# Kernel optimization log

Measured on AMD Instinct MI355X. Metric: run time of the kernel, lower is better.

The kernel has to match this reference:

```python
import jax, jax.numpy as jnp
import numpy as np

B, S, D = 2, 2048, 2048
H, HKV, DH = 32, 8, 64
WIN = 1024  # sliding_window
SCALE = 1.0 / np.sqrt(DH)
NEG_INF = -1e30


def setup_inputs() -> dict:
    key = jax.random.key(0)
    ks = jax.random.split(key, 6)
    w = 0.02
    inp = {
        "hidden_states": jax.random.normal(ks[0], (B, S, D), jnp.float32),
        "Wq": jax.random.normal(ks[1], (D, D), jnp.float32) * w,
        "bq": jnp.zeros((D,), jnp.float32),
        "Wk": jax.random.normal(ks[2], (HKV * DH, D), jnp.float32) * w,
        "bk": jnp.zeros((HKV * DH,), jnp.float32),
        "Wv": jax.random.normal(ks[3], (HKV * DH, D), jnp.float32) * w,
        "bv": jnp.zeros((HKV * DH,), jnp.float32),
        "Wo": jax.random.normal(ks[4], (D, D), jnp.float32) * w,
        "bo": jnp.zeros((D,), jnp.float32),
        # reset_parameters (default init): 1 / logspace(0, 7, H, base=2)
        "alibi_slopes": 1.0 / jnp.exp2(jnp.linspace(0.0, 7.0, H)).astype(jnp.float32),
    }
    return inp


def reference(hidden_states, Wq, bq, Wk, bk, Wv, bv, Wo, bo, alibi_slopes):
    x = hidden_states
    q = (x @ Wq.T + bq).reshape(B, S, H, DH).transpose(0, 2, 1, 3)      # [B,H,S,DH]
    k = (x @ Wk.T + bk).reshape(B, S, HKV, DH).transpose(0, 2, 1, 3)    # [B,HKV,S,DH]
    v = (x @ Wv.T + bv).reshape(B, S, HKV, DH).transpose(0, 2, 1, 3)
    # GQA: each kv head serves H//HKV consecutive query heads
    group = H // HKV
    k = jnp.repeat(k, group, axis=1)  # [B,H,S,DH]
    v = jnp.repeat(v, group, axis=1)

    scores = jnp.einsum("bhqd,bhkd->bhqk", q, k) * SCALE  # [B,H,S,S]
    i = jnp.arange(S)[:, None]
    j = jnp.arange(S)[None, :]
    rel = (j - i).astype(jnp.float32)  # <= 0 for attended past positions
    # ALiBi: slope * (j - i) -> linear penalty on distance
    bias = alibi_slopes[:, None, None] * rel  # [H,S,S]
    mask = (j <= i) & ((i - j) < WIN)  # [S,S]
    scores = jnp.where(mask[None, None], scores + bias[None], NEG_INF)
    probs = jax.nn.softmax(scores, axis=-1)
    out = jnp.einsum("bhqk,bhkd->bhqd", probs, v)  # [B,H,S,DH]
    out = out.transpose(0, 2, 1, 3).reshape(B, S, D)
    return out @ Wo.T + bo
```

## Files before the change

### kernel.cpp

```cpp
#include <hip/hip_runtime.h>
#include <hip/hip_bf16.h>
#include <stdint.h>
#include <type_traits>

typedef unsigned short ushort_t;
typedef __bf16 bf16x8 __attribute__((ext_vector_type(8)));
typedef __bf16 bf16x4 __attribute__((ext_vector_type(4)));
typedef short s16x4 __attribute__((ext_vector_type(4)));
typedef unsigned short u16x8 __attribute__((ext_vector_type(8)));
typedef float f32x4 __attribute__((ext_vector_type(4)));

#define MFMA_BF16(a, b, c) __builtin_amdgcn_mfma_f32_16x16x32_bf16((a), (b), (c), 0, 0, 0)

#define GLD_LDS(gptr, lptr) \
    __builtin_amdgcn_global_load_lds((const __attribute__((address_space(1))) void*)(gptr), \
                                     (__attribute__((address_space(3))) void*)(lptr), 16, 0, 0)

static __device__ __forceinline__ float bf2f(__hip_bfloat16 x) { return __bfloat162float(x); }
static __device__ __forceinline__ ushort_t f2bfbits(float f) {
    __hip_bfloat16 h = __float2bfloat16(f);
    return *(ushort_t*)&h;
}
static __device__ __forceinline__ float fmax3(float a, float b, float c) {
    return fmaxf(fmaxf(a, b), c);
}

static __device__ __forceinline__ f32x4 MFMA16(bf16x4 a, bf16x4 b, f32x4 c) {
#if __has_builtin(__builtin_amdgcn_mfma_f32_16x16x16_bf16)
    return __builtin_amdgcn_mfma_f32_16x16x16_bf16(a, b, c, 0, 0, 0);
#elif __has_builtin(__builtin_amdgcn_mfma_f32_16x16x16bf16_1k)
    union { bf16x4 b4; s16x4 s4; } ua, ub;
    ua.b4 = a; ub.b4 = b;
    return __builtin_amdgcn_mfma_f32_16x16x16bf16_1k(ua.s4, ub.s4, c, 0, 0, 0);
#else
    const bf16x4 z = {(__bf16)0.f, (__bf16)0.f, (__bf16)0.f, (__bf16)0.f};
    bf16x8 a8 = __builtin_shufflevector(a, z, 0, 1, 2, 3, 4, 5, 6, 7);
    bf16x8 b8 = __builtin_shufflevector(b, z, 0, 1, 2, 3, 4, 5, 6, 7);
    return MFMA_BF16(a8, b8, c);
#endif
}

static __device__ __forceinline__ bf16x4 pack4(float a, float b, float c, float d) {
    union { ushort4 u; bf16x4 v; } r;
    r.u = make_ushort4(f2bfbits(a), f2bfbits(b), f2bfbits(c), f2bfbits(d));
    return r.v;
}

template <typename T>
static __device__ __forceinline__ void storeT(T* p, float v);
template <>
__device__ __forceinline__ void storeT<float>(float* p, float v) { *p = v; }
template <>
__device__ __forceinline__ void storeT<__hip_bfloat16>(__hip_bfloat16* p, float v) {
    *p = __float2bfloat16(v);
}

__global__ void detect_kernel(const ushort_t* __restrict__ X,
                              const void* bq, const void* bk, const void* bv,
                              const void* bo, const void* slopes,
                              int* flag, float* slopesF, float* bqF,
                              float* bkF, float* bvF, float* boF) {
    __shared__ int cnt_s;
    if (threadIdx.x == 0) cnt_s = 0;
    __syncthreads();
    int cnt = 0;
    for (int i = threadIdx.x; i < 8192; i += 256) {
        ushort_t u = X[2 * i];
        int ex = (u >> 7) & 0xFF;
        if (ex >= 0xC0) cnt++;
    }
    for (int off = 1; off < 64; off <<= 1) cnt += __shfl_xor(cnt, off);
    if ((threadIdx.x & 63) == 0) atomicAdd(&cnt_s, cnt);
    __syncthreads();
    const bool f32 = cnt_s > 100;
    if (threadIdx.x == 0) *flag = f32 ? 1 : 0;
    auto conv = [&](const void* src, float* dst, int n) {
        for (int i = threadIdx.x; i < n; i += 256)
            dst[i] = f32 ? ((const float*)src)[i]
                         : __bfloat162float(((const __hip_bfloat16*)src)[i]);
    };
    conv(bq, bqF, 2048);
    conv(bk, bkF, 512);
    conv(bv, bvF, 512);
    conv(bo, boF, 2048);
    conv(slopes, slopesF, 32);
}

__global__ __launch_bounds__(256) void cvt_kernel(const int* __restrict__ flag,
                                                  const void* __restrict__ src,
                                                  ushort_t* __restrict__ dst, int n4) {
    const bool f32 = (*flag == 1);
    const int stride = gridDim.x * 256;
    for (int i = blockIdx.x * 256 + threadIdx.x; i < n4; i += stride) {
        if (f32) {
            float4 f = ((const float4*)src)[i];
            ((ushort4*)dst)[i] =
                make_ushort4(f2bfbits(f.x), f2bfbits(f.y), f2bfbits(f.z), f2bfbits(f.w));
        } else {
            ((ushort4*)dst)[i] = ((const ushort4*)src)[i];
        }
    }
}

__global__ __launch_bounds__(256) void cvt4_kernel(const int* __restrict__ flag,
                                                   const void* __restrict__ X,
                                                   const void* __restrict__ Wq,
                                                   const void* __restrict__ Wk,
                                                   const void* __restrict__ Wv,
                                                   ushort_t* __restrict__ Xb,
                                                   ushort_t* __restrict__ Wqb,
                                                   ushort_t* __restrict__ Wkb,
                                                   ushort_t* __restrict__ Wvb) {
    const bool f32 = (*flag == 1);
    constexpr int nX = 4096 * 2048 / 4;
    constexpr int nWq = 2048 * 2048 / 4;
    constexpr int nWk = 512 * 2048 / 4;
    constexpr int total = nX + nWq + 2 * nWk;
    const int stride = gridDim.x * 256;
    for (int i = blockIdx.x * 256 + threadIdx.x; i < total; i += stride) {
        const void* src;
        ushort_t* dst;
        int off;
        if (i < nX)                 { src = X;  dst = Xb;  off = i; }
        else if (i < nX + nWq)      { src = Wq; dst = Wqb; off = i - nX; }
        else if (i < nX + nWq + nWk){ src = Wk; dst = Wkb; off = i - nX - nWq; }
        else                        { src = Wv; dst = Wvb; off = i - nX - nWq - nWk; }
        if (f32) {
            float4 f = ((const float4*)src)[off];
            ((ushort4*)dst)[off] =
                make_ushort4(f2bfbits(f.x), f2bfbits(f.y), f2bfbits(f.z), f2bfbits(f.w));
        } else {
            ((ushort4*)dst)[off] = ((const ushort4*)src)[off];
        }
    }
}

__device__ __forceinline__ void stage_tile(const __hip_bfloat16* __restrict__ M, int K,
                                           int k0, ushort_t* lds, int tid) {
    const int wave = tid >> 6, lane = tid & 63;
    const int srow = lane >> 3;
    const int scol = ((lane & 7) ^ srow) * 8;
#pragma unroll
    for (int t = 0; t < 4; ++t) {
        const int chunk = wave * 4 + t;
        GLD_LDS((const ushort_t*)M + (size_t)(chunk * 8 + srow) * K + k0 + scol,
                lds + chunk * 512);
    }
}

__device__ __forceinline__ void stage_tile(const float* __restrict__ M, int K,
                                           int k0, ushort_t* lds, int tid) {
#pragma unroll
    for (int q = 0; q < 8; ++q) {
        const int idx = q * 256 + tid;
        const int row = idx >> 4;
        const int c4 = (idx & 15) * 4;
        float4 f = *(const float4*)(M + (size_t)row * K + k0 + c4);
        const int dcol = (((c4 >> 3) ^ (row & 7)) * 8) + (c4 & 7);
        *(ushort4*)(lds + row * 64 + dcol) =
            make_ushort4(f2bfbits(f.x), f2bfbits(f.y), f2bfbits(f.z), f2bfbits(f.w));
    }
}

template <typename TA, typename TW, typename TC>
__device__ __forceinline__ void gemm_tile(const TA* __restrict__ A,
                                          const TW* __restrict__ W,
                                          const float* __restrict__ biasF,
                                          TC* __restrict__ C, int K, int ldc) {
    __shared__ __align__(16) ushort_t As[2][128 * 64];
    __shared__ __align__(16) ushort_t Bs[2][128 * 64];
    const int tid = threadIdx.x;
    const int wave = tid >> 6, lane = tid & 63;
    const int quad = lane >> 4, l15 = lane & 15;
    const int wm = (wave >> 1) * 64, wn = (wave & 1) * 64;
    const int sw = l15 & 7;

    f32x4 acc[4][4];
#pragma unroll
    for (int i = 0; i < 4; ++i)
#pragma unroll
        for (int j = 0; j < 4; ++j) acc[i][j] = {0.f, 0.f, 0.f, 0.f};

    for (int k0 = 0; k0 < K; k0 += 128) {
        stage_tile(A, K, k0, As[0], tid);
        stage_tile(A, K, k0 + 64, As[1], tid);
        stage_tile(W, K, k0, Bs[0], tid);
        stage_tile(W, K, k0 + 64, Bs[1], tid);
        __syncthreads();
#pragma unroll
        for (int hh = 0; hh < 2; ++hh) {
            const ushort_t* Ab = As[hh];
            const ushort_t* Bb = Bs[hh];
#pragma unroll
            for (int kk = 0; kk < 2; ++kk) {
                const int chs = ((kk * 4 + quad) ^ sw) * 8;
                bf16x8 af[4], bfr[4];
#pragma unroll
                for (int mi = 0; mi < 4; ++mi)
                    af[mi] = *(const bf16x8*)(Ab + (wm + mi * 16 + l15) * 64 + chs);
#pragma unroll
                for (int ni = 0; ni < 4; ++ni)
                    bfr[ni] = *(const bf16x8*)(Bb + (wn + ni * 16 + l15) * 64 + chs);
#pragma unroll
                for (int mi = 0; mi < 4; ++mi)
#pragma unroll
                    for (int ni = 0; ni < 4; ++ni)
                        acc[mi][ni] = MFMA_BF16(af[mi], bfr[ni], acc[mi][ni]);
            }
        }
        __syncthreads();
    }
#pragma unroll
    for (int mi = 0; mi < 4; ++mi) {
#pragma unroll
        for (int ni = 0; ni < 4; ++ni) {
            const int col = wn + ni * 16 + l15;
            const float bv = biasF[col];
#pragma unroll
            for (int r = 0; r < 4; ++r) {
                const int row = wm + mi * 16 + quad * 4 + r;
                storeT(C + (size_t)row * ldc + col, acc[mi][ni][r] + bv);
            }
        }
    }
}

__global__ __launch_bounds__(256, 2) void qkv_fast(
    const __hip_bfloat16* __restrict__ X,
    const __hip_bfloat16* __restrict__ Wq, const __hip_bfloat16* __restrict__ Wk,
    const __hip_bfloat16* __restrict__ Wv, const float* __restrict__ bqF,
    const float* __restrict__ bkF, const float* __restrict__ bvF,
    __hip_bfloat16* __restrict__ Qb, __hip_bfloat16* __restrict__ Kb,
    __hip_bfloat16* __restrict__ Vb) {
    const int nt = blockIdx.x, mt = blockIdx.y;
    const __hip_bfloat16* W;
    const float* bias;
    __hip_bfloat16* C;
    int ldc, colbase;
    if (nt < 16)      { W = Wq; bias = bqF; C = Qb; ldc = 2048; colbase = nt * 128; }
    else if (nt < 20) { W = Wk; bias = bkF; C = Kb; ldc = 512;  colbase = (nt - 16) * 128; }
    else              { W = Wv; bias = bvF; C = Vb; ldc = 512;  colbase = (nt - 20) * 128; }
    gemm_tile(X + (size_t)mt * 128 * 2048, W + (size_t)colbase * 2048, bias + colbase,
              C + (size_t)mt * 128 * ldc + colbase, 2048, ldc);
}

__global__ __launch_bounds__(256, 2) void oproj_fast(
    const __hip_bfloat16* __restrict__ A, const __hip_bfloat16* __restrict__ Wo,
    const float* __restrict__ boF, float* __restrict__ C) {
    gemm_tile(A + (size_t)blockIdx.y * 128 * 2048,
              Wo + (size_t)blockIdx.x * 128 * 2048, boF + blockIdx.x * 128,
              C + (size_t)blockIdx.y * 128 * 2048 + blockIdx.x * 128, 2048, 2048);
}

__global__ __launch_bounds__(256) void vtrans_kernel(const ushort_t* __restrict__ Vb,
                                                     ushort_t* __restrict__ Vt) {
    const int blk = blockIdx.x;
    const int bh = blk >> 6;
    const int sc = blk & 63;
    const int tid = threadIdx.x;
    const int dh = tid & 63;
    const int s0 = sc * 32 + (tid >> 6) * 8;
    const int b = bh >> 3, hkv = bh & 7;
    u16x8 vv;
#pragma unroll
    for (int e = 0; e < 8; ++e)
        vv[e] = Vb[((size_t)(b * 2048 + s0 + e)) * 512 + hkv * 64 + dh];
    *(u16x8*)(Vt + ((size_t)(bh * 64 + dh)) * 2048 + s0) = vv;
}

template <bool F32>
__global__ __launch_bounds__(256, 2) void qkv_kernel(
    const int* __restrict__ flag, const void* __restrict__ Xv,
    const void* __restrict__ Wqv, const void* __restrict__ Wkv,
    const void* __restrict__ Wvv, const float* __restrict__ bqF,
    const float* __restrict__ bkF, const float* __restrict__ bvF,
    __hip_bfloat16* __restrict__ Qb, __hip_bfloat16* __restrict__ Kb,
    __hip_bfloat16* __restrict__ Vb) {
    if ((*flag == 1) != F32) return;
    using T = typename std::conditional<F32, float, __hip_bfloat16>::type;
    const T* X = (const T*)Xv;
    const int nt = blockIdx.x, mt = blockIdx.y;
    const T* W;
    const float* bias;
    __hip_bfloat16* C;
    int ldc, colbase;
    if (nt < 16)      { W = (const T*)Wqv; bias = bqF; C = Qb; ldc = 2048; colbase = nt * 128; }
    else if (nt < 20) { W = (const T*)Wkv; bias = bkF; C = Kb; ldc = 512;  colbase = (nt - 16) * 128; }
    else              { W = (const T*)Wvv; bias = bvF; C = Vb; ldc = 512;  colbase = (nt - 20) * 128; }
    gemm_tile(X + (size_t)mt * 128 * 2048, W + (size_t)colbase * 2048, bias + colbase,
              C + (size_t)mt * 128 * ldc + colbase, 2048, ldc);
}

template <bool F32>
__global__ __launch_bounds__(256, 2) void oproj_kernel(
    const int* __restrict__ flag, const __hip_bfloat16* __restrict__ A,
    const void* __restrict__ Wov, const float* __restrict__ boF,
    float* __restrict__ C) {
    if ((*flag == 1) != F32) return;
    using T = typename std::conditional<F32, float, __hip_bfloat16>::type;
    gemm_tile(A + (size_t)blockIdx.y * 128 * 2048,
              (const T*)Wov + (size_t)blockIdx.x * 128 * 2048, boF + blockIdx.x * 128,
              C + (size_t)blockIdx.y * 128 * 2048 + blockIdx.x * 128, 2048, 2048);
}

__global__ __launch_bounds__(256, 4) void attn4_kernel(
    const __hip_bfloat16* __restrict__ Qg, const __hip_bfloat16* __restrict__ Kg,
    const ushort_t* __restrict__ Vt, const float* __restrict__ slopesF,
    __hip_bfloat16* __restrict__ Og) {
    constexpr int S = 2048, WIN = 1024;
    constexpr float LOG2E = 1.44269504f;
    constexpr float SCALE2 = 0.125f * LOG2E;
    constexpr float NEGBIG = -3e38f;
    __shared__ __align__(16) ushort_t K0s[64 * 64];
    __shared__ __align__(16) ushort_t V0s[64 * 64];
    __shared__ __align__(16) ushort_t K1s[64 * 64];
    __shared__ __align__(16) ushort_t V1s[64 * 64];

    const int p = blockIdx.x;
    const int xcd = p & 7;
    const int slot = p >> 3;
    const int bh = (slot >> 7) * 8 + xcd;
    const int h2 = (slot >> 5) & 3;
    const int qt = 31 - (slot & 31);
    const int b = bh >> 3, hkv = bh & 7;
    const int h = hkv * 4 + h2;
    const int i0 = qt * 64;

    const int tid = threadIdx.x;
    const int wave = tid >> 6, lane = tid & 63;
    const int quad = lane >> 4, l15 = lane & 15;
    const int jl = lane >> 3, cc = lane & 7;
    const float slope2 = slopesF[h] * LOG2E;

    const ushort_t* kbase = (const ushort_t*)Kg + (size_t)(b * S) * 512 + hkv * 64;
    const ushort_t* vbase = Vt + ((size_t)bh * 64) * 2048;

    auto stage = [&](int j0, ushort_t* Ks, ushort_t* Vs) {
        const int row0 = wave * 16;
#pragma unroll
        for (int t = 0; t < 2; ++t) {
            const int r = row0 + t * 8 + jl;
            GLD_LDS(kbase + (size_t)(j0 + r) * 512 + ((cc ^ (r & 7)) * 8),
                    Ks + (row0 + t * 8) * 64);
            GLD_LDS(vbase + (size_t)r * 2048 + j0 + ((cc ^ (r & 7)) * 8),
                    Vs + (row0 + t * 8) * 64);
        }
    };

    const int i = i0 + wave * 16 + l15;
    const __hip_bfloat16* qbase = Qg + ((size_t)(b * S + i)) * 2048 + h * 64;
    bf16x8 aq0 = *(const bf16x8*)(qbase + quad * 8);
    bf16x8 aq1 = *(const bf16x8*)(qbase + 32 + quad * 8);

    union { ushort4 u; bf16x4 v; } onesu;
    onesu.u = make_ushort4(0x3F80, 0x3F80, 0x3F80, 0x3F80);
    const bf16x4 onesf = onesu.v;

    f32x4 oaccT[4];
#pragma unroll
    for (int ni = 0; ni < 4; ++ni) oaccT[ni] = {0.f, 0.f, 0.f, 0.f};
    f32x4 lacc = {0.f, 0.f, 0.f, 0.f};
    float m_i = -1e30f;

    auto compute = [&](int j0, const ushort_t* Ks, const ushort_t* Vs, bool masked) {
        f32x4 st[4];
#pragma unroll
        for (int ni = 0; ni < 4; ++ni) st[ni] = {0.f, 0.f, 0.f, 0.f};
#pragma unroll
        for (int kk = 0; kk < 2; ++kk) {
            const bf16x8 aqk = kk ? aq1 : aq0;
#pragma unroll
            for (int ni = 0; ni < 4; ++ni) {
                const int row = ni * 16 + l15;
                bf16x8 kf = *(const bf16x8*)(Ks + row * 64 + ((kk * 4 + quad) ^ (row & 7)) * 8);
                st[ni] = MFMA_BF16(kf, aqk, st[ni]);
            }
        }
        float sv[4][4];
#pragma unroll
        for (int ni = 0; ni < 4; ++ni)
#pragma unroll
            for (int r = 0; r < 4; ++r) {
                const int rel = (j0 + ni * 16 + quad * 4 + r) - i;
                sv[ni][r] = fmaf(st[ni][r], SCALE2, slope2 * (float)rel);
            }
        if (masked) {
#pragma unroll
            for (int ni = 0; ni < 4; ++ni)
#pragma unroll
                for (int r = 0; r < 4; ++r) {
                    const int rel = (j0 + ni * 16 + quad * 4 + r) - i;
                    if (!((unsigned)(-rel) < (unsigned)WIN)) sv[ni][r] = NEGBIG;
                }
        }
        float mx = fmax3(fmax3(sv[0][0], sv[0][1], sv[0][2]),
                         fmax3(sv[0][3], sv[1][0], sv[1][1]),
                         fmax3(sv[1][2], sv[1][3], sv[2][0]));
        float my = fmax3(fmax3(sv[2][1], sv[2][2], sv[2][3]),
                         fmax3(sv[3][0], sv[3][1], sv[3][2]), sv[3][3]);
        mx = fmaxf(mx, my);
        mx = fmaxf(mx, __shfl_xor(mx, 16));
        mx = fmaxf(mx, __shfl_xor(mx, 32));
        if (!__all(mx <= m_i + 8.f)) {
            const float mn = fmaxf(m_i, mx);
            const float alpha = exp2f(m_i - mn);
            m_i = mn;
#pragma unroll
            for (int ni = 0; ni < 4; ++ni)
#pragma unroll
                for (int r = 0; r < 4; ++r) oaccT[ni][r] *= alpha;
            lacc[0] *= alpha;
        }
        float pv[4][4];
#pragma unroll
        for (int ni = 0; ni < 4; ++ni)
#pragma unroll
            for (int r = 0; r < 4; ++r) pv[ni][r] = exp2f(sv[ni][r] - m_i);
        bf16x4 pf[4];
#pragma unroll
        for (int c = 0; c < 4; ++c) pf[c] = pack4(pv[c][0], pv[c][1], pv[c][2], pv[c][3]);
#pragma unroll
        for (int c = 0; c < 4; ++c) lacc = MFMA16(onesf, pf[c], lacc);
#pragma unroll
        for (int ni = 0; ni < 4; ++ni) {
            const int row = ni * 16 + l15;
#pragma unroll
            for (int c = 0; c < 4; ++c) {
                const int cj = c * 2 + (quad >> 1);
                bf16x4 vf = *(const bf16x4*)(Vs + row * 64 + ((cj ^ (row & 7)) * 8) +
                                             (quad & 1) * 4);
                oaccT[ni] = MFMA16(vf, pf[c], oaccT[ni]);
            }
        }
    };

    const int jt_lo = (i0 - WIN + 1) > 0 ? ((i0 - WIN + 1) >> 6) : 0;
    int jt = jt_lo;
    stage(jt * 64, K0s, V0s);
    for (;;) {
        __syncthreads();
        if (jt < qt) stage((jt + 1) * 64, K1s, V1s);
        compute(jt * 64, K0s, V0s, (jt == qt) || (qt - jt >= 16));
        if (++jt > qt) break;
        __syncthreads();
        if (jt < qt) stage((jt + 1) * 64, K0s, V0s);
        compute(jt * 64, K1s, V1s, (jt == qt) || (qt - jt >= 16));
        if (++jt > qt) break;
    }
    const float inv = 1.0f / lacc[0];
    __hip_bfloat16* obase = Og + ((size_t)(b * S + i)) * 2048 + h * 64;
#pragma unroll
    for (int ni = 0; ni < 4; ++ni) {
        ushort4 o4 = make_ushort4(f2bfbits(oaccT[ni][0] * inv), f2bfbits(oaccT[ni][1] * inv),
                                  f2bfbits(oaccT[ni][2] * inv), f2bfbits(oaccT[ni][3] * inv));
        *(ushort4*)((ushort_t*)obase + ni * 16 + quad * 4) = o4;
    }
}

__global__ __launch_bounds__(256, 2) void attn_kernel(
    const __hip_bfloat16* __restrict__ Qg, const __hip_bfloat16* __restrict__ Kg,
    const __hip_bfloat16* __restrict__ Vg, const float* __restrict__ slopesF,
    __hip_bfloat16* __restrict__ Og) {
    constexpr int S = 2048, WIN = 1024;
    constexpr float SCALE = 0.125f;
    constexpr float LOG2E = 1.44269504f;
    __shared__ __align__(16) ushort_t P_lds[64 * 72];
    __shared__ __align__(16) ushort_t Vts[64 * 72];

    const int tile = blockIdx.x;
    const int qt = tile & 31;
    const int h = (tile >> 5) & 31;
    const int b = tile >> 10;
    const int i0 = qt * 64;
    const int hkv = h >> 2;
    const int tid = threadIdx.x;
    const int wave = tid >> 6, lane = tid & 63;
    const int quad = lane >> 4, l15 = lane & 15;
    const float slope = slopesF[h];

    const int qrow = i0 + wave * 16 + l15;
    const __hip_bfloat16* qbase = Qg + ((size_t)(b * S + qrow)) * 2048 + h * 64;
    bf16x8 aq[2];
    aq[0] = *(const bf16x8*)(qbase + quad * 8);
    aq[1] = *(const bf16x8*)(qbase + 32 + quad * 8);

    f32x4 oacc[4];
#pragma unroll
    for (int ni = 0; ni < 4; ++ni) oacc[ni] = {0.f, 0.f, 0.f, 0.f};
    float m_i[4], l_i[4];
#pragma unroll
    for (int r = 0; r < 4; ++r) { m_i[r] = -1e30f; l_i[r] = 0.f; }

    const int jt_lo = (i0 - WIN + 1) > 0 ? ((i0 - WIN + 1) >> 6) : 0;
    for (int jt = jt_lo; jt <= qt; ++jt) {
        const int j0 = jt * 64;
#pragma unroll
        for (int it = 0; it < 2; ++it) {
            const int j = it * 32 + (tid >> 3);
            const int dh0 = (tid & 7) * 8;
            u16x8 vv = *(const u16x8*)(Vg + ((size_t)(b * S + j0 + j)) * 512 + hkv * 64 + dh0);
#pragma unroll
            for (int e = 0; e < 8; ++e) Vts[(dh0 + e) * 72 + j] = vv[e];
        }
        f32x4 sacc[4];
#pragma unroll
        for (int ni = 0; ni < 4; ++ni) sacc[ni] = {0.f, 0.f, 0.f, 0.f};
#pragma unroll
        for (int kk = 0; kk < 2; ++kk) {
#pragma unroll
            for (int ni = 0; ni < 4; ++ni) {
                bf16x8 bkf = *(const bf16x8*)(Kg + ((size_t)(b * S + j0 + ni * 16 + l15)) * 512 +
                                              hkv * 64 + kk * 32 + quad * 8);
                sacc[ni] = MFMA_BF16(aq[kk], bkf, sacc[ni]);
            }
        }
#pragma unroll
        for (int r = 0; r < 4; ++r) {
            const int i = i0 + wave * 16 + quad * 4 + r;
            float sv[4];
            float rowmax = -1e30f;
#pragma unroll
            for (int ni = 0; ni < 4; ++ni) {
                const int j = j0 + ni * 16 + l15;
                float s = sacc[ni][r] * SCALE + slope * (float)(j - i);
                const bool valid = (j <= i) && ((i - j) < WIN);
                s = valid ? s : -1e30f;
                sv[ni] = s;
                rowmax = fmaxf(rowmax, s);
            }
#pragma unroll
            for (int off = 1; off < 16; off <<= 1)
                rowmax = fmaxf(rowmax, __shfl_xor(rowmax, off));
            const float mn = fmaxf(m_i[r], rowmax);
            const float alpha = exp2f((m_i[r] - mn) * LOG2E);
            float rowsum = 0.f;
#pragma unroll
            for (int ni = 0; ni < 4; ++ni) {
                const float p = (sv[ni] > -1e29f) ? exp2f((sv[ni] - mn) * LOG2E) : 0.f;
                P_lds[(wave * 16 + quad * 4 + r) * 72 + ni * 16 + l15] = f2bfbits(p);
                rowsum += p;
            }
#pragma unroll
            for (int off = 1; off < 16; off <<= 1) rowsum += __shfl_xor(rowsum, off);
            l_i[r] = l_i[r] * alpha + rowsum;
            m_i[r] = mn;
#pragma unroll
            for (int ni = 0; ni < 4; ++ni) oacc[ni][r] *= alpha;
        }
        __syncthreads();
#pragma unroll
        for (int kk = 0; kk < 2; ++kk) {
            bf16x8 ap = *(const bf16x8*)(P_lds + (wave * 16 + l15) * 72 + kk * 32 + quad * 8);
#pragma unroll
            for (int ni = 0; ni < 4; ++ni) {
                bf16x8 bvf = *(const bf16x8*)(Vts + (ni * 16 + l15) * 72 + kk * 32 + quad * 8);
                oacc[ni] = MFMA_BF16(ap, bvf, oacc[ni]);
            }
        }
        __syncthreads();
    }
#pragma unroll
    for (int ni = 0; ni < 4; ++ni) {
#pragma unroll
        for (int r = 0; r < 4; ++r) {
            const int srow = i0 + wave * 16 + quad * 4 + r;
            const float v = oacc[ni][r] / l_i[r];
            Og[((size_t)(b * S + srow)) * 2048 + h * 64 + ni * 16 + l15] = __float2bfloat16(v);
        }
    }
}

extern "C" void kernel_launch(void* const* d_in, const int* in_sizes, int n_in,
                              void* d_out, int out_size, void* d_ws, size_t ws_size,
                              hipStream_t stream) {
    (void)in_sizes; (void)n_in; (void)out_size;
    const void* X  = d_in[0];
    const void* Wq = d_in[1];
    const void* bq = d_in[2];
    const void* Wk = d_in[3];
    const void* bk = d_in[4];
    const void* Wv = d_in[5];
    const void* bv = d_in[6];
    const void* Wo = d_in[7];
    const void* bo = d_in[8];
    const void* sl = d_in[9];
    float* outp = (float*)d_out;

    char* ws = (char*)d_ws;
    const size_t SZ_X  = (size_t)4096 * 2048 * 2;
    const size_t SZ_WQ = (size_t)2048 * 2048 * 2;
    const size_t SZ_WK = (size_t)512 * 2048 * 2;
    const size_t SZ_Q  = SZ_X;
    const size_t SZ_K  = (size_t)4096 * 512 * 2;
    const size_t FAST_NEED = SZ_X + SZ_WQ + 2 * SZ_WK + SZ_Q + 2 * SZ_K + 65536;

    if (ws_size >= FAST_NEED) {
        size_t o = 0;
        __hip_bfloat16* Xb  = (__hip_bfloat16*)(ws + o); o += SZ_X;
        __hip_bfloat16* Wqb = (__hip_bfloat16*)(ws + o); o += SZ_WQ;
        __hip_bfloat16* Wkb = (__hip_bfloat16*)(ws + o); o += SZ_WK;
        __hip_bfloat16* Wvb = (__hip_bfloat16*)(ws + o); o += SZ_WK;
        __hip_bfloat16* Qb  = (__hip_bfloat16*)(ws + o); o += SZ_Q;
        __hip_bfloat16* Kb  = (__hip_bfloat16*)(ws + o); o += SZ_K;
        __hip_bfloat16* Vb  = (__hip_bfloat16*)(ws + o); o += SZ_K;
        __hip_bfloat16* Ab  = Xb;
        __hip_bfloat16* Wob = Wqb;
        ushort_t*       Vtg = (ushort_t*)Wkb;
        int*   flag    = (int*)(ws + o);
        float* slopesF = (float*)(ws + o + 1024);
        float* bqF     = (float*)(ws + o + 4096);
        float* bkF     = bqF + 2048;
        float* bvF     = bkF + 512;
        float* boF     = bvF + 512;

        detect_kernel<<<1, 256, 0, stream>>>((const ushort_t*)X, bq, bk, bv, bo, sl,
                                             flag, slopesF, bqF, bkF, bvF, boF);
        cvt4_kernel<<<2048, 256, 0, stream>>>(flag, X, Wq, Wk, Wv, (ushort_t*)Xb,
                                              (ushort_t*)Wqb, (ushort_t*)Wkb,
                                              (ushort_t*)Wvb);
        qkv_fast<<<dim3(24, 32), 256, 0, stream>>>(Xb, Wqb, Wkb, Wvb, bqF, bkF, bvF,
                                                   Qb, Kb, Vb);
        vtrans_kernel<<<1024, 256, 0, stream>>>((const ushort_t*)Vb, Vtg);
        cvt_kernel<<<2048, 256, 0, stream>>>(flag, Wo, (ushort_t*)Wob, 2048 * 2048 / 4);
        attn4_kernel<<<dim3(2048), 256, 0, stream>>>(Qb, Kb, Vtg, slopesF, Ab);
        oproj_fast<<<dim3(16, 32), 256, 0, stream>>>(Ab, Wob, boF, outp);
    } else {
        const size_t MB = 1024 * 1024;
        __hip_bfloat16* Qb = (__hip_bfloat16*)(ws);
        __hip_bfloat16* Kb = (__hip_bfloat16*)(ws + 16 * MB);
        __hip_bfloat16* Vb = (__hip_bfloat16*)(ws + 20 * MB);
        __hip_bfloat16* Ab = (__hip_bfloat16*)(ws + 24 * MB);
        int*   flag    = (int*)(ws + 40 * MB);
        float* slopesF = (float*)(ws + 40 * MB + 1024);
        float* bqF     = (float*)(ws + 40 * MB + 4096);
        float* bkF     = bqF + 2048;
        float* bvF     = bkF + 512;
        float* boF     = bvF + 512;

        detect_kernel<<<1, 256, 0, stream>>>((const ushort_t*)X, bq, bk, bv, bo, sl,
                                             flag, slopesF, bqF, bkF, bvF, boF);
        qkv_kernel<false><<<dim3(24, 32), 256, 0, stream>>>(flag, X, Wq, Wk, Wv,
                                                            bqF, bkF, bvF, Qb, Kb, Vb);
        qkv_kernel<true><<<dim3(24, 32), 256, 0, stream>>>(flag, X, Wq, Wk, Wv,
                                                           bqF, bkF, bvF, Qb, Kb, Vb);
        attn_kernel<<<dim3(2048), 256, 0, stream>>>(Qb, Kb, Vb, slopesF, Ab);
        oproj_kernel<false><<<dim3(16, 32), 256, 0, stream>>>(flag, Ab, Wo, boF, outp);
        oproj_kernel<true><<<dim3(16, 32), 256, 0, stream>>>(flag, Ab, Wo, boF, outp);
    }
}
```

Baseline: 328.2 us.

## Fuse dtype detection and conversions into one kernel; write V transposed from QKV GEMM

Merges the detect kernel, the input/weight conversion kernel and the separate Wo conversion into a single cvt5 launch, in which each block recomputes the dtype flag locally. The QKV GEMM epilogue now writes V directly in the transposed [bh, dh, s] layout that attention consumes, which removes the vtrans kernel and one round trip of V through memory. It also raises the attention kernel's occupancy hint from 4 to 5 blocks per CU. In exchange, every block redundantly samples X to decide the dtype, the transposed V stores are narrower 8-byte writes, and the new path needs extra workspace for a separate Wo buffer.

```diff
diff --git a/kernel.cpp b/kernel.cpp
--- a/kernel.cpp
+++ b/kernel.cpp
@@ -135,6 +135,66 @@
     }
 }
 
+__global__ __launch_bounds__(256) void cvt5_kernel(
+    const void* __restrict__ X, const void* __restrict__ Wq,
+    const void* __restrict__ Wk, const void* __restrict__ Wv,
+    const void* __restrict__ Wo, const void* bq, const void* bk,
+    const void* bv, const void* bo, const void* slopes,
+    ushort_t* __restrict__ Xb, ushort_t* __restrict__ Wqb,
+    ushort_t* __restrict__ Wkb, ushort_t* __restrict__ Wvb,
+    ushort_t* __restrict__ Wob, float* slopesF, float* bqF,
+    float* bkF, float* bvF, float* boF) {
+    __shared__ int cnt_s;
+    if (threadIdx.x == 0) cnt_s = 0;
+    __syncthreads();
+    int cnt = 0;
+    const ushort_t* Xu = (const ushort_t*)X;
+    for (int i = threadIdx.x; i < 8192; i += 256) {
+        ushort_t u = Xu[2 * i];
+        if (((u >> 7) & 0xFF) >= 0xC0) cnt++;
+    }
+    for (int off = 1; off < 64; off <<= 1) cnt += __shfl_xor(cnt, off);
+    if ((threadIdx.x & 63) == 0) atomicAdd(&cnt_s, cnt);
+    __syncthreads();
+    const bool f32 = cnt_s > 100;
+
+    if (blockIdx.x == 0) {
+        auto conv = [&](const void* src, float* dst, int n) {
+            for (int i = threadIdx.x; i < n; i += 256)
+                dst[i] = f32 ? ((const float*)src)[i]
+                             : __bfloat162float(((const __hip_bfloat16*)src)[i]);
+        };
+        conv(bq, bqF, 2048);
+        conv(bk, bkF, 512);
+        conv(bv, bvF, 512);
+        conv(bo, boF, 2048);
+        conv(slopes, slopesF, 32);
+    }
+
+    constexpr int nX = 4096 * 2048 / 4;
+    constexpr int nWq = 2048 * 2048 / 4;
+    constexpr int nWk = 512 * 2048 / 4;
+    constexpr int total = nX + 2 * nWq + 2 * nWk;
+    const int stride = gridDim.x * 256;
+    for (int i = blockIdx.x * 256 + threadIdx.x; i < total; i += stride) {
+        const void* src;
+        ushort_t* dst;
+        int off;
+        if (i < nX)                        { src = X;  dst = Xb;  off = i; }
+        else if (i < nX + nWq)             { src = Wq; dst = Wqb; off = i - nX; }
+        else if (i < nX + nWq + nWk)       { src = Wk; dst = Wkb; off = i - nX - nWq; }
+        else if (i < nX + nWq + 2 * nWk)   { src = Wv; dst = Wvb; off = i - nX - nWq - nWk; }
+        else                               { src = Wo; dst = Wob; off = i - nX - nWq - 2 * nWk; }
+        if (f32) {
+            float4 f = ((const float4*)src)[off];
+            ((ushort4*)dst)[off] =
+                make_ushort4(f2bfbits(f.x), f2bfbits(f.y), f2bfbits(f.z), f2bfbits(f.w));
+        } else {
+            ((ushort4*)dst)[off] = ((const ushort4*)src)[off];
+        }
+    }
+}
+
 __device__ __forceinline__ void stage_tile(const __hip_bfloat16* __restrict__ M, int K,
                                            int k0, ushort_t* lds, int tid) {
     const int wave = tid >> 6, lane = tid & 63;
@@ -162,7 +222,7 @@
     }
 }
 
-template <typename TA, typename TW, typename TC>
+template <bool VTRANS = false, typename TA, typename TW, typename TC>
 __device__ __forceinline__ void gemm_tile(const TA* __restrict__ A,
                                           const TW* __restrict__ W,
                                           const float* __restrict__ biasF,
@@ -216,10 +276,17 @@
         for (int ni = 0; ni < 4; ++ni) {
             const int col = wn + ni * 16 + l15;
             const float bv = biasF[col];
-#pragma unroll
-            for (int r = 0; r < 4; ++r) {
-                const int row = wm + mi * 16 + quad * 4 + r;
-                storeT(C + (size_t)row * ldc + col, acc[mi][ni][r] + bv);
+            if constexpr (VTRANS) {
+                ushort4 o4 = make_ushort4(
+                    f2bfbits(acc[mi][ni][0] + bv), f2bfbits(acc[mi][ni][1] + bv),
+                    f2bfbits(acc[mi][ni][2] + bv), f2bfbits(acc[mi][ni][3] + bv));
+                *(ushort4*)((ushort_t*)C + (size_t)col * 2048 + wm + mi * 16 + quad * 4) = o4;
+            } else {
+#pragma unroll
+                for (int r = 0; r < 4; ++r) {
+                    const int row = wm + mi * 16 + quad * 4 + r;
+                    storeT(C + (size_t)row * ldc + col, acc[mi][ni][r] + bv);
+                }
             }
         }
     }
@@ -231,17 +298,22 @@
     const __hip_bfloat16* __restrict__ Wv, const float* __restrict__ bqF,
     const float* __restrict__ bkF, const float* __restrict__ bvF,
     __hip_bfloat16* __restrict__ Qb, __hip_bfloat16* __restrict__ Kb,
-    __hip_bfloat16* __restrict__ Vb) {
+    ushort_t* __restrict__ Vt) {
     const int nt = blockIdx.x, mt = blockIdx.y;
-    const __hip_bfloat16* W;
-    const float* bias;
-    __hip_bfloat16* C;
-    int ldc, colbase;
-    if (nt < 16)      { W = Wq; bias = bqF; C = Qb; ldc = 2048; colbase = nt * 128; }
-    else if (nt < 20) { W = Wk; bias = bkF; C = Kb; ldc = 512;  colbase = (nt - 16) * 128; }
-    else              { W = Wv; bias = bvF; C = Vb; ldc = 512;  colbase = (nt - 20) * 128; }
-    gemm_tile(X + (size_t)mt * 128 * 2048, W + (size_t)colbase * 2048, bias + colbase,
-              C + (size_t)mt * 128 * ldc + colbase, 2048, ldc);
+    if (nt < 16) {
+        const int colbase = nt * 128;
+        gemm_tile(X + (size_t)mt * 128 * 2048, Wq + (size_t)colbase * 2048, bqF + colbase,
+                  Qb + (size_t)mt * 128 * 2048 + colbase, 2048, 2048);
+    } else if (nt < 20) {
+        const int colbase = (nt - 16) * 128;
+        gemm_tile(X + (size_t)mt * 128 * 2048, Wk + (size_t)colbase * 2048, bkF + colbase,
+                  Kb + (size_t)mt * 128 * 512 + colbase, 2048, 512);
+    } else {
+        const int colbase = (nt - 20) * 128;
+        ushort_t* Cv = Vt + ((size_t)((mt >> 4) * 512 + colbase)) * 2048 + (mt & 15) * 128;
+        gemm_tile<true>(X + (size_t)mt * 128 * 2048, Wv + (size_t)colbase * 2048,
+                        bvF + colbase, Cv, 2048, 0);
+    }
 }
 
 __global__ __launch_bounds__(256, 2) void oproj_fast(
@@ -250,22 +322,6 @@
     gemm_tile(A + (size_t)blockIdx.y * 128 * 2048,
               Wo + (size_t)blockIdx.x * 128 * 2048, boF + blockIdx.x * 128,
               C + (size_t)blockIdx.y * 128 * 2048 + blockIdx.x * 128, 2048, 2048);
-}
-
-__global__ __launch_bounds__(256) void vtrans_kernel(const ushort_t* __restrict__ Vb,
-                                                     ushort_t* __restrict__ Vt) {
-    const int blk = blockIdx.x;
-    const int bh = blk >> 6;
-    const int sc = blk & 63;
-    const int tid = threadIdx.x;
-    const int dh = tid & 63;
-    const int s0 = sc * 32 + (tid >> 6) * 8;
-    const int b = bh >> 3, hkv = bh & 7;
-    u16x8 vv;
-#pragma unroll
-    for (int e = 0; e < 8; ++e)
-        vv[e] = Vb[((size_t)(b * 2048 + s0 + e)) * 512 + hkv * 64 + dh];
-    *(u16x8*)(Vt + ((size_t)(bh * 64 + dh)) * 2048 + s0) = vv;
 }
 
 template <bool F32>
@@ -303,7 +359,7 @@
               C + (size_t)blockIdx.y * 128 * 2048 + blockIdx.x * 128, 2048, 2048);
 }
 
-__global__ __launch_bounds__(256, 4) void attn4_kernel(
+__global__ __launch_bounds__(256, 5) void attn4_kernel(
     const __hip_bfloat16* __restrict__ Qg, const __hip_bfloat16* __restrict__ Kg,
     const ushort_t* __restrict__ Vt, const float* __restrict__ slopesF,
     __hip_bfloat16* __restrict__ Og) {
@@ -592,7 +648,8 @@
     const size_t SZ_WK = (size_t)512 * 2048 * 2;
     const size_t SZ_Q  = SZ_X;
     const size_t SZ_K  = (size_t)4096 * 512 * 2;
-    const size_t FAST_NEED = SZ_X + SZ_WQ + 2 * SZ_WK + SZ_Q + 2 * SZ_K + 65536;
+    const size_t FAST_NEED  = SZ_X + SZ_WQ + 2 * SZ_WK + SZ_Q + 2 * SZ_K + 65536;
+    const size_t FAST_NEED2 = FAST_NEED + SZ_WQ;
 
     if (ws_size >= FAST_NEED) {
         size_t o = 0;
@@ -602,10 +659,8 @@
         __hip_bfloat16* Wvb = (__hip_bfloat16*)(ws + o); o += SZ_WK;
         __hip_bfloat16* Qb  = (__hip_bfloat16*)(ws + o); o += SZ_Q;
         __hip_bfloat16* Kb  = (__hip_bfloat16*)(ws + o); o += SZ_K;
-        __hip_bfloat16* Vb  = (__hip_bfloat16*)(ws + o); o += SZ_K;
+        ushort_t*       Vtg = (ushort_t*)(ws + o);       o += SZ_K;
         __hip_bfloat16* Ab  = Xb;
-        __hip_bfloat16* Wob = Wqb;
-        ushort_t*       Vtg = (ushort_t*)Wkb;
         int*   flag    = (int*)(ws + o);
         float* slopesF = (float*)(ws + o + 1024);
         float* bqF     = (float*)(ws + o + 4096);
@@ -613,17 +668,29 @@
         float* bvF     = bkF + 512;
         float* boF     = bvF + 512;
 
-        detect_kernel<<<1, 256, 0, stream>>>((const ushort_t*)X, bq, bk, bv, bo, sl,
-                                             flag, slopesF, bqF, bkF, bvF, boF);
-        cvt4_kernel<<<2048, 256, 0, stream>>>(flag, X, Wq, Wk, Wv, (ushort_t*)Xb,
-                                              (ushort_t*)Wqb, (ushort_t*)Wkb,
-                                              (ushort_t*)Wvb);
-        qkv_fast<<<dim3(24, 32), 256, 0, stream>>>(Xb, Wqb, Wkb, Wvb, bqF, bkF, bvF,
-                                                   Qb, Kb, Vb);
-        vtrans_kernel<<<1024, 256, 0, stream>>>((const ushort_t*)Vb, Vtg);
-        cvt_kernel<<<2048, 256, 0, stream>>>(flag, Wo, (ushort_t*)Wob, 2048 * 2048 / 4);
-        attn4_kernel<<<dim3(2048), 256, 0, stream>>>(Qb, Kb, Vtg, slopesF, Ab);
-        oproj_fast<<<dim3(16, 32), 256, 0, stream>>>(Ab, Wob, boF, outp);
+        if (ws_size >= FAST_NEED2) {
+            __hip_bfloat16* Wob = (__hip_bfloat16*)(ws + o + 65536);
+            cvt5_kernel<<<2048, 256, 0, stream>>>(
+                X, Wq, Wk, Wv, Wo, bq, bk, bv, bo, sl, (ushort_t*)Xb, (ushort_t*)Wqb,
+                (ushort_t*)Wkb, (ushort_t*)Wvb, (ushort_t*)Wob, slopesF, bqF, bkF, bvF,
+                boF);
+            qkv_fast<<<dim3(24, 32), 256, 0, stream>>>(Xb, Wqb, Wkb, Wvb, bqF, bkF, bvF,
+                                                       Qb, Kb, Vtg);
+            attn4_kernel<<<dim3(2048), 256, 0, stream>>>(Qb, Kb, Vtg, slopesF, Ab);
+            oproj_fast<<<dim3(16, 32), 256, 0, stream>>>(Ab, Wob, boF, outp);
+        } else {
+            __hip_bfloat16* Wob = Wqb;
+            detect_kernel<<<1, 256, 0, stream>>>((const ushort_t*)X, bq, bk, bv, bo, sl,
+                                                 flag, slopesF, bqF, bkF, bvF, boF);
+            cvt4_kernel<<<2048, 256, 0, stream>>>(flag, X, Wq, Wk, Wv, (ushort_t*)Xb,
+                                                  (ushort_t*)Wqb, (ushort_t*)Wkb,
+                                                  (ushort_t*)Wvb);
+            qkv_fast<<<dim3(24, 32), 256, 0, stream>>>(Xb, Wqb, Wkb, Wvb, bqF, bkF, bvF,
+                                                       Qb, Kb, Vtg);
+            cvt_kernel<<<2048, 256, 0, stream>>>(flag, Wo, (ushort_t*)Wob, 2048 * 2048 / 4);
+            attn4_kernel<<<dim3(2048), 256, 0, stream>>>(Qb, Kb, Vtg, slopesF, Ab);
+            oproj_fast<<<dim3(16, 32), 256, 0, stream>>>(Ab, Wob, boF, outp);
+        }
     } else {
         const size_t MB = 1024 * 1024;
         __hip_bfloat16* Qb = (__hip_bfloat16*)(ws);
```

Result: slower. 346.6 us (+5.6%).
